# Kernel tuning notes

Hardware: AMD Instinct MI355X
Metric: run time of the kernel (lower is better)

## Reference

```python
import jax, jax.numpy as jnp
import numpy as np

B, S, DIN, DH = 8, 8192, 256, 256


def setup_inputs() -> dict:
    key = jax.random.key(0)
    k0, k1, k2, k3, k4 = jax.random.split(key, 5)
    stdv = 1.0 / np.sqrt(DIN)
    x = jax.random.normal(k0, (B, S, DIN), jnp.float32)
    W0 = jax.random.uniform(k1, (2 * DH, DIN), jnp.float32, -stdv, stdv)
    b0 = jax.random.uniform(k2, (2 * DH,), jnp.float32, -stdv, stdv)
    stdv2 = 1.0 / np.sqrt(DH)
    W1 = jax.random.uniform(k3, (2 * DH, DH), jnp.float32, -stdv2, stdv2)
    b1 = jax.random.uniform(k4, (2 * DH,), jnp.float32, -stdv2, stdv2)
    return {"x": x, "W0": W0, "b0": b0, "W1": W1, "b1": b1}


def _log_g(x):
    # log of g(x) = x + 0.5 for x >= 0 else sigmoid(x)
    return jnp.where(x >= 0, jnp.log(jax.nn.relu(x) + 0.5), -jax.nn.softplus(-x))


def _mingru_layer(x, W, b):
    # x: (B,S,Din); W: (2*DH, Din); b: (2*DH,)
    gh = jnp.einsum('bsd,ed->bse', x, W) + b          # (B,S,2*DH)
    gate, hidden = jnp.split(gh, 2, axis=-1)          # each (B,S,DH)
    log_coeffs = -jax.nn.softplus(gate)               # log(1 - z)
    log_vals = -jax.nn.softplus(-gate) + _log_g(hidden)  # log z + log h_tilde
    Bb, Ss, Dd = log_coeffs.shape
    # initial hidden h0 = g(0) = 0.5  ->  log(h0) = log(0.5)
    log_h0 = jnp.full((Bb, 1, Dd), jnp.log(0.5), log_coeffs.dtype)
    log_values = jnp.concatenate([log_h0, log_vals], axis=1)          # (B,S+1,DH)
    a_star = jnp.concatenate(
        [jnp.zeros((Bb, 1, Dd), log_coeffs.dtype), jnp.cumsum(log_coeffs, axis=1)],
        axis=1)                                                       # (B,S+1,DH)
    log_h = a_star + jax.lax.cumlogsumexp(log_values - a_star, axis=1)
    return jnp.exp(log_h)[:, 1:]                                      # (B,S,DH)


def reference(x, W0, b0, W1, b1):
    out0 = _mingru_layer(x, W0, b0)
    out1 = _mingru_layer(out0, W1, b1)
    h = jnp.stack([out0[:, -1:], out1[:, -1:]])  # (num_layers,B,1,DH)
    return out1, h
```

## Files before the change

kernel.cpp:

```cpp
#include <hip/hip_runtime.h>
#include <hip/hip_bf16.h>

#define Bb 8
#define Ss 8192
#define Dd 256
#define Mm (Bb * Ss)
#define Nn 512
#define NCHUNK 128
#define CLEN (Ss / NCHUNK)
#define TSP 68

typedef __hip_bfloat16 bf16;
typedef __attribute__((ext_vector_type(8))) short short8;
typedef __attribute__((ext_vector_type(4))) float f32x4;

__device__ __forceinline__ void load_lds16(const void* g, void* l) {
  __builtin_amdgcn_global_load_lds(
      (const __attribute__((address_space(1))) void*)g,
      (__attribute__((address_space(3))) void*)l, 16, 0, 0);
}

template <int N>
__device__ __forceinline__ void wait_vmcnt() {
  if constexpr (N == 0)
    asm volatile("s_waitcnt vmcnt(0)" ::: "memory");
  else if constexpr (N == 4)
    asm volatile("s_waitcnt vmcnt(4)" ::: "memory");
  else if constexpr (N == 6)
    asm volatile("s_waitcnt vmcnt(6)" ::: "memory");
  else
    static_assert(N == 0 || N == 4 || N == 6, "unsupported vmcnt");
}

__global__ __launch_bounds__(256) void cvt_weights(
    const float* __restrict__ inA, const float* __restrict__ inB,
    bf16* __restrict__ outA, bf16* __restrict__ outB, long n4each) {
  long i = (long)blockIdx.x * blockDim.x + threadIdx.x;
  const float* in = inA;
  bf16* out = outA;
  if (i >= n4each) {
    in = inB;
    out = outB;
    i -= n4each;
  }
  if (i >= n4each) return;
  const float4 v = ((const float4*)in)[i];
  union { ushort4 u; bf16 h[4]; } o;
  o.h[0] = __float2bfloat16(v.x);
  o.h[1] = __float2bfloat16(v.y);
  o.h[2] = __float2bfloat16(v.z);
  o.h[3] = __float2bfloat16(v.w);
  ((ushort4*)out)[i] = o.u;
}

__device__ __forceinline__ void av_from_gh(float gate, float hid, float& a,
                                           float& v) {
  gate = fminf(fmaxf(gate, -20.f), 20.f);
  float eg = __expf(gate);
  a = 1.f / (1.f + eg);
  float z = eg * a;
  float eh = __expf(fminf(fmaxf(hid, -20.f), 0.f));
  float sig = eh / (1.f + eh);
  float gfun = (hid >= 0.f) ? (hid + 0.5f) : sig;
  v = z * gfun;
}

__device__ __forceinline__ unsigned pack_av(float a, float v) {
  union { bf16 h[2]; unsigned u; } o;
  o.h[0] = __float2bfloat16(a);
  o.h[1] = __float2bfloat16(v);
  return o.u;
}

template <bool F32A>
__global__ __launch_bounds__(256, F32A ? 3 : 5) void gemm_av_fused(
    const void* __restrict__ Xv, const bf16* __restrict__ W,
    const float* __restrict__ bias, unsigned* __restrict__ AV,
    float2* __restrict__ AVs) {
  constexpr int ABY = F32A ? 16384 : 8192;
  constexpr int NLD = F32A ? 6 : 4;
  __shared__ __align__(16) char sm[2 * ABY + 16384];
  char* Ab[2] = {sm, sm + ABY};
  bf16* Bbf[2] = {(bf16*)(sm + 2 * ABY), (bf16*)(sm + 2 * ABY + 8192)};
  unsigned* Ts = (unsigned*)sm;

  const int tid = threadIdx.x;
  const int w = tid >> 6;
  const int l = tid & 63;
  const int fl = l & 15;
  const int q = l >> 4;

  const int id = blockIdx.x;
  const int lin = ((id & 7) << 8) | (id >> 3);
  const int cb = lin & 3;
  const int bt = lin >> 2;
  const long rowBase = (long)bt * 128;
  const int wrow = (w >> 1) * 64;
  const int wc = (w & 1) * 32;

  const float* Xf = (const float*)Xv;
  const bf16* Xb = (const bf16*)Xv;

  const float* aSrcF[4];
  const bf16* aSrcB[2];
  const bf16* bSrc[2];
  int aDstF[4], sDst[2];
  if constexpr (F32A) {
#pragma unroll
    for (int c = 0; c < 4; c++) {
      const int L = c * 256 + tid;
      const int row = L >> 3;
      const int kc = (L & 7) ^ (row & 7);
      aSrcF[c] = Xf + (rowBase + row) * 256 + kc * 4;
      aDstF[c] = (c * 256 + w * 64) * 16;
    }
  } else {
#pragma unroll
    for (int c = 0; c < 2; c++) {
      const int L = c * 256 + tid;
      const int row = L >> 2;
      const int kc = (L & 3) ^ ((row >> 1) & 3);
      aSrcB[c] = Xb + (rowBase + row) * 256 + kc * 8;
    }
  }
#pragma unroll
  for (int c = 0; c < 2; c++) {
    const int L = c * 256 + tid;
    const int row = L >> 2;
    const int kc = (L & 3) ^ ((row >> 1) & 3);
    const int grow = (row < 64) ? (cb * 64 + row) : (192 + cb * 64 + row);
    bSrc[c] = W + (long)grow * 256 + kc * 8;
    sDst[c] = (c * 256 + w * 64) * 16;
  }
  auto stage = [&](int bi, int ks) {
    if constexpr (F32A) {
#pragma unroll
      for (int c = 0; c < 4; c++)
        load_lds16(aSrcF[c] + ks * 32, Ab[bi] + aDstF[c]);
    } else {
#pragma unroll
      for (int c = 0; c < 2; c++)
        load_lds16(aSrcB[c] + ks * 32, Ab[bi] + sDst[c]);
    }
#pragma unroll
    for (int c = 0; c < 2; c++)
      load_lds16(bSrc[c] + ks * 32, (char*)Bbf[bi] + sDst[c]);
  };

  auto fragA = [&](const char* buf, int mt) -> short8 {
    const int row = wrow + 16 * mt + fl;
    if constexpr (F32A) {
      const float* p = (const float*)buf + row * 32;
      const int k0c = (2 * q) ^ (row & 7);
      const int k1c = (2 * q + 1) ^ (row & 7);
      const float4 u0 = *(const float4*)(p + k0c * 4);
      const float4 u1 = *(const float4*)(p + k1c * 4);
      const float vals[8] = {u0.x, u0.y, u0.z, u0.w, u1.x, u1.y, u1.z, u1.w};
      short8 r;
#pragma unroll
      for (int i = 0; i < 8; i++) {
        union { bf16 h; short s; } t;
        t.h = __float2bfloat16(vals[i]);
        r[i] = t.s;
      }
      return r;
    } else {
      const int kc = q ^ ((row >> 1) & 3);
      return *(const short8*)((const bf16*)buf + row * 32 + kc * 8);
    }
  };
  auto fragB = [&](const bf16* buf, int nt) -> short8 {
    const int row =
        (nt < 2) ? (wc + 16 * nt + fl) : (64 + wc + 16 * (nt - 2) + fl);
    const int kc = q ^ ((row >> 1) & 3);
    return *(const short8*)(buf + row * 32 + kc * 8);
  };

  f32x4 acc[4][4];
#pragma unroll
  for (int i = 0; i < 4; i++)
#pragma unroll
    for (int j = 0; j < 4; j++) acc[i][j] = (f32x4)0.0f;

  stage(0, 0);
  stage(1, 1);
#pragma unroll
  for (int ks = 0; ks < 8; ks++) {
    const int bi = ks & 1;
    if (ks < 7)
      wait_vmcnt<NLD>();
    else
      wait_vmcnt<0>();
    __builtin_amdgcn_s_barrier();
    __builtin_amdgcn_sched_barrier(0);
    short8 af[4], bf_[4];
#pragma unroll
    for (int mt = 0; mt < 4; mt++) af[mt] = fragA(Ab[bi], mt);
#pragma unroll
    for (int nt = 0; nt < 4; nt++) bf_[nt] = fragB(Bbf[bi], nt);
#pragma unroll
    for (int mt = 0; mt < 4; mt++)
#pragma unroll
      for (int nt = 0; nt < 4; nt++)
        acc[mt][nt] = __builtin_amdgcn_mfma_f32_16x16x32_bf16(
            af[mt], bf_[nt], acc[mt][nt], 0, 0, 0);
    asm volatile("s_waitcnt lgkmcnt(0)" ::: "memory");
    __builtin_amdgcn_s_barrier();
    __builtin_amdgcn_sched_barrier(0);
    if (ks < 6) stage(bi, ks + 2);
  }

  float bg[2], bh[2];
#pragma unroll
  for (int p = 0; p < 2; p++) {
    const int d = cb * 64 + wc + 16 * p + fl;
    bg[p] = bias[d];
    bh[p] = bias[256 + d];
  }
  unsigned pk[4][2][4];
#pragma unroll
  for (int mt = 0; mt < 4; mt++)
#pragma unroll
    for (int p = 0; p < 2; p++)
#pragma unroll
      for (int r = 0; r < 4; r++) {
        float a, v;
        av_from_gh(acc[mt][p][r] + bg[p], acc[mt][p + 2][r] + bh[p], a, v);
        pk[mt][p][r] = pack_av(a, v);
      }

#pragma unroll
  for (int h = 0; h < 2; h++) {
    if ((w >> 1) == h) {
#pragma unroll
      for (int mt = 0; mt < 4; mt++)
#pragma unroll
        for (int p = 0; p < 2; p++)
#pragma unroll
          for (int r = 0; r < 4; r++)
            Ts[(16 * mt + 4 * q + r) * TSP + wc + 16 * p + fl] = pk[mt][p][r];
    }
    __syncthreads();
    {
      unsigned* dst = AV + ((long)cb * Mm + rowBase + h * 64) * 64;
#pragma unroll
      for (int j = 0; j < 4; j++) {
        const int idx = j * 256 + tid;
        const int t = idx >> 4;
        const int d4 = idx & 15;
        const uint4 val = *(const uint4*)(Ts + t * TSP + d4 * 4);
        *(uint4*)(dst + 4 * idx) = val;
      }
    }
    if (tid < 64) {
      float A = 1.f, H = 0.f;
#pragma unroll 8
      for (int t = 0; t < 64; t++) {
        const unsigned p = Ts[t * TSP + tid];
        const float a = __uint_as_float((p & 0xffffu) << 16);
        const float v = __uint_as_float(p & 0xffff0000u);
        A *= a;
        H = a * H + v;
      }
      const long cg = (long)(bt >> 6) * NCHUNK + ((bt & 63) << 1) + h;
      AVs[cg * 256 + cb * 64 + tid] = make_float2(A, H);
    }
    __syncthreads();
  }
}

template <bool WRITE_BF16>
__global__ __launch_bounds__(256) void scan_final(
    const unsigned* __restrict__ AV, const float2* __restrict__ AVs,
    bf16* __restrict__ OutB, float* __restrict__ OutF,
    float* __restrict__ Hlast) {
  const int d = threadIdx.x;
  const int c = blockIdx.x % NCHUNK;
  const int b = blockIdx.x / NCHUNK;

  float h = 0.5f;
#pragma unroll 4
  for (int j = 0; j < c; j++) {
    const float2 av = AVs[((long)b * NCHUNK + j) * 256 + d];
    h = av.x * h + av.y;
  }

  const long row0 = (long)b * Ss + (long)c * CLEN;
  const unsigned* src = AV + (long)(d >> 6) * Mm * 64 + (d & 63);
  long obase = row0 * 256 + d;
#pragma unroll 8
  for (int t = 0; t < CLEN; t++) {
    const unsigned p = src[(row0 + t) * 64];
    const float a = __uint_as_float((p & 0xffffu) << 16);
    const float v = __uint_as_float(p & 0xffff0000u);
    h = a * h + v;
    if (WRITE_BF16)
      OutB[obase] = __float2bfloat16(h);
    else
      OutF[obase] = h;
    obase += 256;
  }
  if (c == NCHUNK - 1) Hlast[b * 256 + d] = h;
}

extern "C" void kernel_launch(void* const* d_in, const int* in_sizes, int n_in,
                              void* d_out, int out_size, void* d_ws,
                              size_t ws_size, hipStream_t stream) {
  const float* x = (const float*)d_in[0];
  const float* W0f = (const float*)d_in[1];
  const float* b0 = (const float*)d_in[2];
  const float* W1f = (const float*)d_in[3];
  const float* b1 = (const float*)d_in[4];

  float* outF = (float*)d_out;
  float* hlast = outF + (long)Mm * 256;
  bf16* X1b = (bf16*)d_out;

  char* ws = (char*)d_ws;
  unsigned* AV = (unsigned*)ws;
  bf16* W0b = (bf16*)(ws + (long)Mm * 256 * 4);
  bf16* W1b = W0b + (long)Nn * Dd;
  float2* AVs = (float2*)(W1b + (long)Nn * Dd);

  const dim3 gemmGrid(2048);
  const dim3 blk(256);

  const long n4w = (long)Nn * Dd / 4;
  cvt_weights<<<dim3((2 * n4w + 255) / 256), blk, 0, stream>>>(W0f, W1f, W0b,
                                                               W1b, n4w);

  gemm_av_fused<true><<<gemmGrid, blk, 0, stream>>>(x, W0b, b0, AV, AVs);
  scan_final<true><<<dim3(Bb * NCHUNK), blk, 0, stream>>>(AV, AVs, X1b,
                                                          nullptr, hlast);

  gemm_av_fused<false><<<gemmGrid, blk, 0, stream>>>(X1b, W1b, b1, AV, AVs);
  scan_final<false><<<dim3(Bb * NCHUNK), blk, 0, stream>>>(
      AV, AVs, nullptr, outF, hlast + Bb * 256);
}
```

Before: 277.5 us.

## Keep full-K weight tile resident in LDS and stream A fragments directly to registers

The GEMM is restructured so each block loads its entire 64x256 weight slice into LDS once. Each wave then reads its A fragments straight from global memory into registers with register double-buffering, replacing the per-K-step LDS staging and the barriers around it. Column tiles shrink from 64 to 32 features per block, so the grid doubles and the AV workspace layout changes to 32-wide groups, with the scan kernel updated to match. This removes per-step synchronisation and LDS traffic for A. In exchange each X row tile is now read by twice as many blocks, and uncoalesced per-lane global loads may add latency.

```diff
diff --git a/kernel.cpp b/kernel.cpp
--- a/kernel.cpp
+++ b/kernel.cpp
@@ -8,7 +8,7 @@
 #define Nn 512
 #define NCHUNK 128
 #define CLEN (Ss / NCHUNK)
-#define TSP 68
+#define TSW 36
 
 typedef __hip_bfloat16 bf16;
 typedef __attribute__((ext_vector_type(8))) short short8;
@@ -18,18 +18,6 @@
   __builtin_amdgcn_global_load_lds(
       (const __attribute__((address_space(1))) void*)g,
       (__attribute__((address_space(3))) void*)l, 16, 0, 0);
-}
-
-template <int N>
-__device__ __forceinline__ void wait_vmcnt() {
-  if constexpr (N == 0)
-    asm volatile("s_waitcnt vmcnt(0)" ::: "memory");
-  else if constexpr (N == 4)
-    asm volatile("s_waitcnt vmcnt(4)" ::: "memory");
-  else if constexpr (N == 6)
-    asm volatile("s_waitcnt vmcnt(6)" ::: "memory");
-  else
-    static_assert(N == 0 || N == 4 || N == 6, "unsupported vmcnt");
 }
 
 __global__ __launch_bounds__(256) void cvt_weights(
@@ -73,15 +61,12 @@
 }
 
 template <bool F32A>
-__global__ __launch_bounds__(256, F32A ? 3 : 5) void gemm_av_fused(
+__global__ __launch_bounds__(256, F32A ? 3 : 4) void gemm_av_fused(
     const void* __restrict__ Xv, const bf16* __restrict__ W,
     const float* __restrict__ bias, unsigned* __restrict__ AV,
     float2* __restrict__ AVs) {
-  constexpr int ABY = F32A ? 16384 : 8192;
-  constexpr int NLD = F32A ? 6 : 4;
-  __shared__ __align__(16) char sm[2 * ABY + 16384];
-  char* Ab[2] = {sm, sm + ABY};
-  bf16* Bbf[2] = {(bf16*)(sm + 2 * ABY), (bf16*)(sm + 2 * ABY + 8192)};
+  __shared__ __align__(16) char sm[32768];
+  bf16* Bs = (bf16*)sm;
   unsigned* Ts = (unsigned*)sm;
 
   const int tid = threadIdx.x;
@@ -91,70 +76,74 @@
   const int q = l >> 4;
 
   const int id = blockIdx.x;
-  const int lin = ((id & 7) << 8) | (id >> 3);
-  const int cb = lin & 3;
-  const int bt = lin >> 2;
+  const int lin = ((id & 7) << 9) | (id >> 3);
+  const int cb = lin & 7;
+  const int bt = lin >> 3;
   const long rowBase = (long)bt * 128;
-  const int wrow = (w >> 1) * 64;
-  const int wc = (w & 1) * 32;
+
+  {
+#pragma unroll
+    for (int it = 0; it < 8; it++) {
+      const int L = it * 256 + tid;
+      const int row = L >> 5;
+      const int kc = (L & 31) ^ (row & 7);
+      const int grow =
+          (row < 32) ? (cb * 32 + row) : (256 + cb * 32 + (row - 32));
+      load_lds16(W + (long)grow * 256 + kc * 8,
+                 (char*)sm + (it * 256 + w * 64) * 16);
+    }
+  }
+  asm volatile("s_waitcnt vmcnt(0)" ::: "memory");
+  __syncthreads();
 
   const float* Xf = (const float*)Xv;
   const bf16* Xb = (const bf16*)Xv;
-
-  const float* aSrcF[4];
-  const bf16* aSrcB[2];
-  const bf16* bSrc[2];
-  int aDstF[4], sDst[2];
-  if constexpr (F32A) {
-#pragma unroll
-    for (int c = 0; c < 4; c++) {
-      const int L = c * 256 + tid;
-      const int row = L >> 3;
-      const int kc = (L & 7) ^ (row & 7);
-      aSrcF[c] = Xf + (rowBase + row) * 256 + kc * 4;
-      aDstF[c] = (c * 256 + w * 64) * 16;
-    }
-  } else {
-#pragma unroll
-    for (int c = 0; c < 2; c++) {
-      const int L = c * 256 + tid;
-      const int row = L >> 2;
-      const int kc = (L & 3) ^ ((row >> 1) & 3);
-      aSrcB[c] = Xb + (rowBase + row) * 256 + kc * 8;
-    }
-  }
-#pragma unroll
-  for (int c = 0; c < 2; c++) {
-    const int L = c * 256 + tid;
-    const int row = L >> 2;
-    const int kc = (L & 3) ^ ((row >> 1) & 3);
-    const int grow = (row < 64) ? (cb * 64 + row) : (192 + cb * 64 + row);
-    bSrc[c] = W + (long)grow * 256 + kc * 8;
-    sDst[c] = (c * 256 + w * 64) * 16;
-  }
-  auto stage = [&](int bi, int ks) {
+  const float* aPF[2];
+  const bf16* aPB[2];
+#pragma unroll
+  for (int mt = 0; mt < 2; mt++) {
+    const long arow = rowBase + w * 32 + 16 * mt + fl;
+    aPF[mt] = Xf + arow * 256 + q * 8;
+    aPB[mt] = Xb + arow * 256 + q * 8;
+  }
+  const int bswz = fl & 7;
+  int bRow[4];
+#pragma unroll
+  for (int nt = 0; nt < 4; nt++) bRow[nt] = (nt * 16 + fl) * 256;
+
+  f32x4 acc[2][4];
+#pragma unroll
+  for (int i = 0; i < 2; i++)
+#pragma unroll
+    for (int j = 0; j < 4; j++) acc[i][j] = (f32x4)0.0f;
+
+  short8 aB_[2][2];
+  float4 aR[2][2][2];
+  short8 bF[2][4];
+
+  auto loadA = [&](int bi, int ks) {
     if constexpr (F32A) {
 #pragma unroll
-      for (int c = 0; c < 4; c++)
-        load_lds16(aSrcF[c] + ks * 32, Ab[bi] + aDstF[c]);
+      for (int mt = 0; mt < 2; mt++) {
+        aR[bi][mt][0] = *(const float4*)(aPF[mt] + ks * 32);
+        aR[bi][mt][1] = *(const float4*)(aPF[mt] + ks * 32 + 4);
+      }
     } else {
 #pragma unroll
-      for (int c = 0; c < 2; c++)
-        load_lds16(aSrcB[c] + ks * 32, Ab[bi] + sDst[c]);
-    }
-#pragma unroll
-    for (int c = 0; c < 2; c++)
-      load_lds16(bSrc[c] + ks * 32, (char*)Bbf[bi] + sDst[c]);
+      for (int mt = 0; mt < 2; mt++)
+        aB_[bi][mt] = *(const short8*)(aPB[mt] + ks * 32);
+    }
   };
-
-  auto fragA = [&](const char* buf, int mt) -> short8 {
-    const int row = wrow + 16 * mt + fl;
+  auto loadB = [&](int bi, int ks) {
+#pragma unroll
+    for (int nt = 0; nt < 4; nt++)
+      bF[bi][nt] =
+          *(const short8*)(Bs + bRow[nt] + (((ks * 4 + q) ^ bswz) * 8));
+  };
+  auto getA = [&](int bi, int mt) -> short8 {
     if constexpr (F32A) {
-      const float* p = (const float*)buf + row * 32;
-      const int k0c = (2 * q) ^ (row & 7);
-      const int k1c = (2 * q + 1) ^ (row & 7);
-      const float4 u0 = *(const float4*)(p + k0c * 4);
-      const float4 u1 = *(const float4*)(p + k1c * 4);
+      const float4 u0 = aR[bi][mt][0];
+      const float4 u1 = aR[bi][mt][1];
       const float vals[8] = {u0.x, u0.y, u0.z, u0.w, u1.x, u1.y, u1.z, u1.w};
       short8 r;
 #pragma unroll
@@ -165,61 +154,40 @@
       }
       return r;
     } else {
-      const int kc = q ^ ((row >> 1) & 3);
-      return *(const short8*)((const bf16*)buf + row * 32 + kc * 8);
+      return aB_[bi][mt];
     }
   };
-  auto fragB = [&](const bf16* buf, int nt) -> short8 {
-    const int row =
-        (nt < 2) ? (wc + 16 * nt + fl) : (64 + wc + 16 * (nt - 2) + fl);
-    const int kc = q ^ ((row >> 1) & 3);
-    return *(const short8*)(buf + row * 32 + kc * 8);
-  };
-
-  f32x4 acc[4][4];
-#pragma unroll
-  for (int i = 0; i < 4; i++)
-#pragma unroll
-    for (int j = 0; j < 4; j++) acc[i][j] = (f32x4)0.0f;
-
-  stage(0, 0);
-  stage(1, 1);
+
+  loadA(0, 0);
+  loadB(0, 0);
 #pragma unroll
   for (int ks = 0; ks < 8; ks++) {
     const int bi = ks & 1;
-    if (ks < 7)
-      wait_vmcnt<NLD>();
-    else
-      wait_vmcnt<0>();
-    __builtin_amdgcn_s_barrier();
-    __builtin_amdgcn_sched_barrier(0);
-    short8 af[4], bf_[4];
-#pragma unroll
-    for (int mt = 0; mt < 4; mt++) af[mt] = fragA(Ab[bi], mt);
-#pragma unroll
-    for (int nt = 0; nt < 4; nt++) bf_[nt] = fragB(Bbf[bi], nt);
-#pragma unroll
-    for (int mt = 0; mt < 4; mt++)
-#pragma unroll
-      for (int nt = 0; nt < 4; nt++)
-        acc[mt][nt] = __builtin_amdgcn_mfma_f32_16x16x32_bf16(
-            af[mt], bf_[nt], acc[mt][nt], 0, 0, 0);
-    asm volatile("s_waitcnt lgkmcnt(0)" ::: "memory");
-    __builtin_amdgcn_s_barrier();
-    __builtin_amdgcn_sched_barrier(0);
-    if (ks < 6) stage(bi, ks + 2);
+    if (ks < 7) {
+      loadA(bi ^ 1, ks + 1);
+      loadB(bi ^ 1, ks + 1);
+    }
+    const short8 a0 = getA(bi, 0);
+    const short8 a1 = getA(bi, 1);
+#pragma unroll
+    for (int nt = 0; nt < 4; nt++) {
+      acc[0][nt] = __builtin_amdgcn_mfma_f32_16x16x32_bf16(a0, bF[bi][nt],
+                                                           acc[0][nt], 0, 0, 0);
+      acc[1][nt] = __builtin_amdgcn_mfma_f32_16x16x32_bf16(a1, bF[bi][nt],
+                                                           acc[1][nt], 0, 0, 0);
+    }
   }
 
   float bg[2], bh[2];
 #pragma unroll
   for (int p = 0; p < 2; p++) {
-    const int d = cb * 64 + wc + 16 * p + fl;
+    const int d = cb * 32 + 16 * p + fl;
     bg[p] = bias[d];
     bh[p] = bias[256 + d];
   }
-  unsigned pk[4][2][4];
-#pragma unroll
-  for (int mt = 0; mt < 4; mt++)
+  unsigned pk[2][2][4];
+#pragma unroll
+  for (int mt = 0; mt < 2; mt++)
 #pragma unroll
     for (int p = 0; p < 2; p++)
 #pragma unroll
@@ -229,43 +197,42 @@
         pk[mt][p][r] = pack_av(a, v);
       }
 
-#pragma unroll
-  for (int h = 0; h < 2; h++) {
-    if ((w >> 1) == h) {
-#pragma unroll
-      for (int mt = 0; mt < 4; mt++)
-#pragma unroll
-        for (int p = 0; p < 2; p++)
-#pragma unroll
-          for (int r = 0; r < 4; r++)
-            Ts[(16 * mt + 4 * q + r) * TSP + wc + 16 * p + fl] = pk[mt][p][r];
-    }
-    __syncthreads();
-    {
-      unsigned* dst = AV + ((long)cb * Mm + rowBase + h * 64) * 64;
-#pragma unroll
-      for (int j = 0; j < 4; j++) {
-        const int idx = j * 256 + tid;
-        const int t = idx >> 4;
-        const int d4 = idx & 15;
-        const uint4 val = *(const uint4*)(Ts + t * TSP + d4 * 4);
-        *(uint4*)(dst + 4 * idx) = val;
-      }
-    }
-    if (tid < 64) {
-      float A = 1.f, H = 0.f;
+  __syncthreads();
+
+#pragma unroll
+  for (int mt = 0; mt < 2; mt++)
+#pragma unroll
+    for (int p = 0; p < 2; p++)
+#pragma unroll
+      for (int r = 0; r < 4; r++)
+        Ts[(w * 32 + 16 * mt + 4 * q + r) * TSW + 16 * p + fl] =
+            pk[mt][p][r];
+  __syncthreads();
+
+  {
+    unsigned* dst = AV + ((long)cb * Mm + rowBase) * 32;
+#pragma unroll
+    for (int it = 0; it < 4; it++) {
+      const int idx = it * 256 + tid;
+      const int t = idx >> 3;
+      const int d4 = idx & 7;
+      *(uint4*)(dst + t * 32 + d4 * 4) = *(const uint4*)(Ts + t * TSW + d4 * 4);
+    }
+  }
+
+  if (tid < 64) {
+    const int h = tid >> 5;
+    const int dl = tid & 31;
+    float A = 1.f, H = 0.f;
 #pragma unroll 8
-      for (int t = 0; t < 64; t++) {
-        const unsigned p = Ts[t * TSP + tid];
-        const float a = __uint_as_float((p & 0xffffu) << 16);
-        const float v = __uint_as_float(p & 0xffff0000u);
-        A *= a;
-        H = a * H + v;
-      }
-      const long cg = (long)(bt >> 6) * NCHUNK + ((bt & 63) << 1) + h;
-      AVs[cg * 256 + cb * 64 + tid] = make_float2(A, H);
-    }
-    __syncthreads();
+    for (int t = 0; t < 64; t++) {
+      const unsigned p = Ts[(64 * h + t) * TSW + dl];
+      const float a = __uint_as_float((p & 0xffffu) << 16);
+      const float v = __uint_as_float(p & 0xffff0000u);
+      A *= a;
+      H = a * H + v;
+    }
+    AVs[((long)bt * 2 + h) * 256 + cb * 32 + dl] = make_float2(A, H);
   }
 }
 
@@ -286,11 +253,11 @@
   }
 
   const long row0 = (long)b * Ss + (long)c * CLEN;
-  const unsigned* src = AV + (long)(d >> 6) * Mm * 64 + (d & 63);
+  const unsigned* src = AV + (long)(d >> 5) * Mm * 32 + (d & 31);
   long obase = row0 * 256 + d;
 #pragma unroll 8
   for (int t = 0; t < CLEN; t++) {
-    const unsigned p = src[(row0 + t) * 64];
+    const unsigned p = src[(row0 + t) * 32];
     const float a = __uint_as_float((p & 0xffffu) << 16);
     const float v = __uint_as_float(p & 0xffff0000u);
     h = a * h + v;
@@ -322,7 +289,7 @@
   bf16* W1b = W0b + (long)Nn * Dd;
   float2* AVs = (float2*)(W1b + (long)Nn * Dd);
 
-  const dim3 gemmGrid(2048);
+  const dim3 gemmGrid(4096);
   const dim3 blk(256);
 
   const long n4w = (long)Nn * Dd / 4;
```

New measurement: 299.4 us. 1.08x slower.

## Replace direct global-to-LDS loads with register-staged prefetch and bf16 LDS tiles

Applied to the files above, without the earlier changes.

Drops the global_load_lds async copies and instead prefetches the next K-slice into registers, converts fp32 activations to bf16 before writing them to LDS, and writes the following buffer while the current one is consumed. The fp32 A tile shrinks to half its LDS size, the conversion happens once per element at staging rather than inside fragment loads, and launch bounds are unified at 3. The costs are more registers, an extra register-to-LDS write pass, and reliance on compiler scheduling now that the explicit vmcnt waits and sched barriers are gone. The occupancy hint for the bf16 variant also drops from 5 to 3.

```diff
diff --git a/kernel.cpp b/kernel.cpp
--- a/kernel.cpp
+++ b/kernel.cpp
@@ -13,24 +13,6 @@
 typedef __hip_bfloat16 bf16;
 typedef __attribute__((ext_vector_type(8))) short short8;
 typedef __attribute__((ext_vector_type(4))) float f32x4;
-
-__device__ __forceinline__ void load_lds16(const void* g, void* l) {
-  __builtin_amdgcn_global_load_lds(
-      (const __attribute__((address_space(1))) void*)g,
-      (__attribute__((address_space(3))) void*)l, 16, 0, 0);
-}
-
-template <int N>
-__device__ __forceinline__ void wait_vmcnt() {
-  if constexpr (N == 0)
-    asm volatile("s_waitcnt vmcnt(0)" ::: "memory");
-  else if constexpr (N == 4)
-    asm volatile("s_waitcnt vmcnt(4)" ::: "memory");
-  else if constexpr (N == 6)
-    asm volatile("s_waitcnt vmcnt(6)" ::: "memory");
-  else
-    static_assert(N == 0 || N == 4 || N == 6, "unsupported vmcnt");
-}
 
 __global__ __launch_bounds__(256) void cvt_weights(
     const float* __restrict__ inA, const float* __restrict__ inB,
@@ -73,15 +55,13 @@
 }
 
 template <bool F32A>
-__global__ __launch_bounds__(256, F32A ? 3 : 5) void gemm_av_fused(
+__global__ __launch_bounds__(256, 3) void gemm_av_fused(
     const void* __restrict__ Xv, const bf16* __restrict__ W,
     const float* __restrict__ bias, unsigned* __restrict__ AV,
     float2* __restrict__ AVs) {
-  constexpr int ABY = F32A ? 16384 : 8192;
-  constexpr int NLD = F32A ? 6 : 4;
-  __shared__ __align__(16) char sm[2 * ABY + 16384];
-  char* Ab[2] = {sm, sm + ABY};
-  bf16* Bbf[2] = {(bf16*)(sm + 2 * ABY), (bf16*)(sm + 2 * ABY + 8192)};
+  __shared__ __align__(16) char sm[32768];
+  bf16* Ab[2] = {(bf16*)sm, (bf16*)(sm + 8192)};
+  bf16* Bbf[2] = {(bf16*)(sm + 16384), (bf16*)(sm + 24576)};
   unsigned* Ts = (unsigned*)sm;
 
   const int tid = threadIdx.x;
@@ -101,80 +81,76 @@
   const float* Xf = (const float*)Xv;
   const bf16* Xb = (const bf16*)Xv;
 
-  const float* aSrcF[4];
-  const bf16* aSrcB[2];
-  const bf16* bSrc[2];
-  int aDstF[4], sDst[2];
-  if constexpr (F32A) {
-#pragma unroll
-    for (int c = 0; c < 4; c++) {
-      const int L = c * 256 + tid;
-      const int row = L >> 3;
-      const int kc = (L & 7) ^ (row & 7);
-      aSrcF[c] = Xf + (rowBase + row) * 256 + kc * 4;
-      aDstF[c] = (c * 256 + w * 64) * 16;
-    }
-  } else {
+  const float* aSF[2];
+  const bf16* aSB[2];
+  const bf16* bS[2];
+  int ldsOff[2];
+#pragma unroll
+  for (int c = 0; c < 2; c++) {
+    const int idx = c * 256 + tid;
+    const int row = idx >> 2;
+    const int kq = idx & 3;
+    ldsOff[c] = row * 32 + (kq ^ ((row >> 1) & 3)) * 8;
+    aSF[c] = Xf + (rowBase + row) * 256 + kq * 8;
+    aSB[c] = Xb + (rowBase + row) * 256 + kq * 8;
+    const int grow = (row < 64) ? (cb * 64 + row) : (192 + cb * 64 + row);
+    bS[c] = W + (long)grow * 256 + kq * 8;
+  }
+
+  short8 aReg[2], bReg[2];
+  float4 aF[2][2];
+
+  auto loadG = [&](int ks) {
+    if constexpr (F32A) {
+#pragma unroll
+      for (int c = 0; c < 2; c++) {
+        aF[c][0] = *(const float4*)(aSF[c] + ks * 32);
+        aF[c][1] = *(const float4*)(aSF[c] + ks * 32 + 4);
+      }
+    } else {
+#pragma unroll
+      for (int c = 0; c < 2; c++)
+        aReg[c] = *(const short8*)(aSB[c] + ks * 32);
+    }
+#pragma unroll
+    for (int c = 0; c < 2; c++)
+      bReg[c] = *(const short8*)(bS[c] + ks * 32);
+  };
+  auto writeL = [&](int bi) {
 #pragma unroll
     for (int c = 0; c < 2; c++) {
-      const int L = c * 256 + tid;
-      const int row = L >> 2;
-      const int kc = (L & 3) ^ ((row >> 1) & 3);
-      aSrcB[c] = Xb + (rowBase + row) * 256 + kc * 8;
-    }
-  }
-#pragma unroll
-  for (int c = 0; c < 2; c++) {
-    const int L = c * 256 + tid;
-    const int row = L >> 2;
-    const int kc = (L & 3) ^ ((row >> 1) & 3);
-    const int grow = (row < 64) ? (cb * 64 + row) : (192 + cb * 64 + row);
-    bSrc[c] = W + (long)grow * 256 + kc * 8;
-    sDst[c] = (c * 256 + w * 64) * 16;
-  }
-  auto stage = [&](int bi, int ks) {
-    if constexpr (F32A) {
-#pragma unroll
-      for (int c = 0; c < 4; c++)
-        load_lds16(aSrcF[c] + ks * 32, Ab[bi] + aDstF[c]);
-    } else {
-#pragma unroll
-      for (int c = 0; c < 2; c++)
-        load_lds16(aSrcB[c] + ks * 32, Ab[bi] + sDst[c]);
+      short8 av_;
+      if constexpr (F32A) {
+        const float vals[8] = {aF[c][0].x, aF[c][0].y, aF[c][0].z, aF[c][0].w,
+                               aF[c][1].x, aF[c][1].y, aF[c][1].z, aF[c][1].w};
+#pragma unroll
+        for (int i = 0; i < 8; i++) {
+          union { bf16 h; short s; } t;
+          t.h = __float2bfloat16(vals[i]);
+          av_[i] = t.s;
+        }
+      } else {
+        av_ = aReg[c];
+      }
+      *(short8*)(Ab[bi] + ldsOff[c]) = av_;
     }
 #pragma unroll
     for (int c = 0; c < 2; c++)
-      load_lds16(bSrc[c] + ks * 32, (char*)Bbf[bi] + sDst[c]);
+      *(short8*)(Bbf[bi] + ldsOff[c]) = bReg[c];
   };
 
-  auto fragA = [&](const char* buf, int mt) -> short8 {
+  int aOff[4], bOff[4];
+#pragma unroll
+  for (int mt = 0; mt < 4; mt++) {
     const int row = wrow + 16 * mt + fl;
-    if constexpr (F32A) {
-      const float* p = (const float*)buf + row * 32;
-      const int k0c = (2 * q) ^ (row & 7);
-      const int k1c = (2 * q + 1) ^ (row & 7);
-      const float4 u0 = *(const float4*)(p + k0c * 4);
-      const float4 u1 = *(const float4*)(p + k1c * 4);
-      const float vals[8] = {u0.x, u0.y, u0.z, u0.w, u1.x, u1.y, u1.z, u1.w};
-      short8 r;
-#pragma unroll
-      for (int i = 0; i < 8; i++) {
-        union { bf16 h; short s; } t;
-        t.h = __float2bfloat16(vals[i]);
-        r[i] = t.s;
-      }
-      return r;
-    } else {
-      const int kc = q ^ ((row >> 1) & 3);
-      return *(const short8*)((const bf16*)buf + row * 32 + kc * 8);
-    }
-  };
-  auto fragB = [&](const bf16* buf, int nt) -> short8 {
+    aOff[mt] = row * 32 + (q ^ ((row >> 1) & 3)) * 8;
+  }
+#pragma unroll
+  for (int nt = 0; nt < 4; nt++) {
     const int row =
         (nt < 2) ? (wc + 16 * nt + fl) : (64 + wc + 16 * (nt - 2) + fl);
-    const int kc = q ^ ((row >> 1) & 3);
-    return *(const short8*)(buf + row * 32 + kc * 8);
-  };
+    bOff[nt] = row * 32 + (q ^ ((row >> 1) & 3)) * 8;
+  }
 
   f32x4 acc[4][4];
 #pragma unroll
@@ -182,22 +158,22 @@
 #pragma unroll
     for (int j = 0; j < 4; j++) acc[i][j] = (f32x4)0.0f;
 
-  stage(0, 0);
-  stage(1, 1);
+  loadG(0);
+  writeL(0);
+  loadG(1);
+  __syncthreads();
 #pragma unroll
   for (int ks = 0; ks < 8; ks++) {
     const int bi = ks & 1;
-    if (ks < 7)
-      wait_vmcnt<NLD>();
-    else
-      wait_vmcnt<0>();
-    __builtin_amdgcn_s_barrier();
-    __builtin_amdgcn_sched_barrier(0);
     short8 af[4], bf_[4];
 #pragma unroll
-    for (int mt = 0; mt < 4; mt++) af[mt] = fragA(Ab[bi], mt);
-#pragma unroll
-    for (int nt = 0; nt < 4; nt++) bf_[nt] = fragB(Bbf[bi], nt);
+    for (int mt = 0; mt < 4; mt++)
+      af[mt] = *(const short8*)(Ab[bi] + aOff[mt]);
+#pragma unroll
+    for (int nt = 0; nt < 4; nt++)
+      bf_[nt] = *(const short8*)(Bbf[bi] + bOff[nt]);
+    if (ks < 7) writeL(bi ^ 1);
+    if (ks < 6) loadG(ks + 2);
 #pragma unroll
     for (int mt = 0; mt < 4; mt++)
 #pragma unroll
@@ -206,8 +182,6 @@
             af[mt], bf_[nt], acc[mt][nt], 0, 0, 0);
     asm volatile("s_waitcnt lgkmcnt(0)" ::: "memory");
     __builtin_amdgcn_s_barrier();
-    __builtin_amdgcn_sched_barrier(0);
-    if (ks < 6) stage(bi, ks + 2);
   }
 
   float bg[2], bh[2];
```

Result: faster. 264.5 us (-4.7%).
